# Optimization experiments

Hardware: AMD Instinct MI355X
Metric: run time of the kernel (lower is better)

Reference implementation:

```python
import jax, jax.numpy as jnp
import numpy as np

N_NODES = 50000
N_HEDGES = 50000
NNZ = 1_600_000
IN_CH = 256      # hedge feature dim
OUT_CH = 256
NODE_CH = 128    # node feature dim
Q_CH = 64        # query_channels
NEG_SLOPE = 0.2


def _glorot(key, shape):
    fan_in, fan_out = shape
    lim = np.sqrt(6.0 / (fan_in + fan_out)).astype(np.float32)
    return jax.random.uniform(key, shape, jnp.float32, -lim, lim)


def setup_inputs() -> dict:
    key = jax.random.key(0)
    ks = jax.random.split(key, 10)
    p = jax.random.normal(ks[0], (N_NODES, NODE_CH), jnp.float32)
    q = jax.random.normal(ks[1], (N_HEDGES, IN_CH), jnp.float32)
    node_idx = jax.random.randint(ks[2], (NNZ,), 0, N_NODES)
    hedge_idx = jax.random.randint(ks[3], (NNZ,), 0, N_HEDGES)
    hedge_index = jnp.stack([node_idx, hedge_idx]).astype(jnp.int64)
    w1 = _glorot(ks[4], (IN_CH, NODE_CH))
    w2 = _glorot(ks[5], (IN_CH, Q_CH))
    w3 = _glorot(ks[6], (NODE_CH, Q_CH))
    w4 = _glorot(ks[7], (NODE_CH, OUT_CH))
    w5 = _glorot(ks[8], (NODE_CH, Q_CH))
    w6 = _glorot(ks[9], (IN_CH, Q_CH))
    return {"p": p, "q": q, "hedge_index": hedge_index,
            "w1": w1, "w2": w2, "w3": w3, "w4": w4, "w5": w5, "w6": w6}


def _segment_softmax(scores, seg, num_segments):
    # PyG-style: exp(x - segment_max) / (segment_sum + 1e-16)
    m = jax.lax.stop_gradient(jax.ops.segment_max(scores, seg, num_segments=num_segments))
    ex = jnp.exp(scores - m[seg])
    s = jax.ops.segment_sum(ex, seg, num_segments=num_segments)
    return ex / (s[seg] + 1e-16)


def reference(p, q, hedge_index, w1, w2, w3, w4, w5, w6):
    n_nodes, n_hedges = p.shape[0], q.shape[0]
    node_i = hedge_index[0]   # [E] node ids
    hedge_j = hedge_index[1]  # [E] hedge ids
    scale = 1.0 / np.sqrt(Q_CH).astype(np.float32)

    # --- stage 1: hedge -> node attention ---
    q_p = q @ w1              # [H, node_ch]
    q_pp = q @ w2             # [H, Q]
    q_ppp = p @ w3            # [N, Q]
    e = jax.nn.leaky_relu((q_ppp[node_i] * q_pp[hedge_j]).sum(-1), NEG_SLOPE)
    e = _segment_softmax(e, node_i, n_nodes)
    p_out = jax.ops.segment_sum(scale * e[:, None] * q_p[hedge_j], node_i,
                                num_segments=n_nodes)  # [N, node_ch]

    # --- stage 2: node -> hedge attention ---
    p_p = p_out @ w4          # [N, out_ch]
    p_pp = p_out @ w5         # [N, Q]
    p_ppp = q @ w6            # [H, Q]
    v = jax.nn.leaky_relu((p_pp[node_i] * p_ppp[hedge_j]).sum(-1), NEG_SLOPE)
    v = _segment_softmax(v, hedge_j, n_hedges)
    q_out = jax.ops.segment_sum(scale * v[:, None] * p_p[node_i], hedge_j,
                                num_segments=n_hedges)  # [H, out_ch]
    return q_out
```

## Files before the change

kernel.cpp:

```cpp
#include <hip/hip_runtime.h>
#include <hip/hip_bf16.h>

#define NODE_CH 128
#define IN_CH   256
#define OUT_CH  256
#define Q_CH    64
#define MAXD    256

#define W_BITS 7
#define W_SEG  128
#define MAX_NB 400
#define CAP    4608
#define CHUNK  4096

__device__ __forceinline__ int load_idx(const void* base, long long i, int is64) {
  if (is64) return (int)((const long long*)base)[i];
  return ((const int*)base)[i];
}

__global__ void detect_kernel(const unsigned int* __restrict__ idx, int* __restrict__ flag) {
  if (threadIdx.x == 0 && blockIdx.x == 0) {
    int allz = 1;
    for (int i = 1; i < 32; i += 2) allz &= (idx[i] == 0u);
    *flag = allz;
  }
}

__global__ __launch_bounds__(512) void bin_kernel(
    const void* __restrict__ idx, const int* __restrict__ flagp,
    int* __restrict__ stagingN, int* __restrict__ stagingH,
    int* __restrict__ gbcntN, int* __restrict__ gbcntH,
    long long E, int NBN, int NBH) {
  __shared__ int ni[CHUNK], hj[CHUNK];
  __shared__ int histN[MAX_NB], histH[MAX_NB];
  __shared__ int baseN[MAX_NB], baseH[MAX_NB];
  __shared__ int curN[MAX_NB],  curH[MAX_NB];
  int is64 = *flagp;
  long long e0 = (long long)blockIdx.x * CHUNK;
  int n = (int)((E - e0 < CHUNK) ? (E - e0) : CHUNK);
  for (int i = threadIdx.x; i < n; i += 512) {
    ni[i] = load_idx(idx, e0 + i, is64);
    hj[i] = load_idx(idx, E + e0 + i, is64);
  }
  for (int i = threadIdx.x; i < MAX_NB; i += 512) {
    histN[i] = 0; histH[i] = 0; curN[i] = 0; curH[i] = 0;
  }
  __syncthreads();
  for (int i = threadIdx.x; i < n; i += 512) {
    atomicAdd(&histN[ni[i] >> W_BITS], 1);
    atomicAdd(&histH[hj[i] >> W_BITS], 1);
  }
  __syncthreads();
  for (int b = threadIdx.x; b < NBN; b += 512)
    if (histN[b]) baseN[b] = atomicAdd(&gbcntN[b], histN[b]);
  for (int b = threadIdx.x; b < NBH; b += 512)
    if (histH[b]) baseH[b] = atomicAdd(&gbcntH[b], histH[b]);
  __syncthreads();
  for (int i = threadIdx.x; i < n; i += 512) {
    int v = ni[i], h = hj[i];
    int bn = v >> W_BITS, bh = h >> W_BITS;
    int rn = baseN[bn] + atomicAdd(&curN[bn], 1);
    if (rn < CAP) stagingN[bn * CAP + rn] = ((v & (W_SEG - 1)) << 16) | h;
    int rh = baseH[bh] + atomicAdd(&curH[bh], 1);
    if (rh < CAP) stagingH[bh * CAP + rh] = ((h & (W_SEG - 1)) << 16) | v;
  }
}

__global__ __launch_bounds__(512) void bucket_sort_kernel(
    const int* __restrict__ stagingN, const int* __restrict__ gbcntN,
    int* __restrict__ rowN, int* __restrict__ csrN, int SN, int NBN,
    const int* __restrict__ stagingH, const int* __restrict__ gbcntH,
    int* __restrict__ rowH, int* __restrict__ csrH, int SH, int NBH,
    long long E) {
  int side = blockIdx.y;
  const int* staging = side ? stagingH : stagingN;
  const int* gbcnt   = side ? gbcntH   : gbcntN;
  int* row = side ? rowH : rowN;
  int* csr = side ? csrH : csrN;
  int S  = side ? SH  : SN;
  int NB = side ? NBH : NBN;
  int b = blockIdx.x;
  if (b >= NB) return;

  __shared__ int eLDS[CAP];
  __shared__ int outb[CAP];
  __shared__ int hist[W_SEG], lstart[W_SEG + 1], cnt[W_SEG];
  __shared__ int red[8];
  __shared__ int basesh;

  int n_b = gbcnt[b];
  int nc = (n_b < CAP) ? n_b : CAP;

  int partial = 0;
  for (int i = threadIdx.x; i < b; i += 512) partial += gbcnt[i];
  #pragma unroll
  for (int o = 1; o < 64; o <<= 1) partial += __shfl_xor(partial, o);
  if ((threadIdx.x & 63) == 0) red[threadIdx.x >> 6] = partial;
  for (int i = threadIdx.x; i < W_SEG; i += 512) { hist[i] = 0; cnt[i] = 0; }
  __syncthreads();
  if (threadIdx.x == 0) {
    int s = 0;
    #pragma unroll
    for (int w = 0; w < 8; ++w) s += red[w];
    basesh = s;
  }
  __syncthreads();
  int base = basesh;

  for (int i = threadIdx.x; i < nc; i += 512) {
    int e = staging[b * CAP + i];
    eLDS[i] = e;
    atomicAdd(&hist[e >> 16], 1);
  }
  __syncthreads();
  if (threadIdx.x == 0) {
    int acc = 0;
    for (int s = 0; s < W_SEG; ++s) { lstart[s] = acc; acc += hist[s]; }
    lstart[W_SEG] = acc;
  }
  __syncthreads();
  int s0 = b * W_SEG;
  for (int s = threadIdx.x; s < W_SEG; s += 512)
    if (s0 + s < S) row[s0 + s] = base + lstart[s];
  if (b == NB - 1 && threadIdx.x == 0) row[S] = (int)E;
  __syncthreads();
  for (int i = threadIdx.x; i < nc; i += 512) {
    int e = eLDS[i];
    int s = e >> 16;
    int r = atomicAdd(&cnt[s], 1);
    outb[lstart[s] + r] = e & 0xffff;
  }
  __syncthreads();
  for (int i = threadIdx.x; i < nc; i += 512) csr[base + i] = outb[i];
}

#define GBM 128
#define GBN 64
#define GBK 16

__device__ __forceinline__ unsigned short f2bf(float f) {
  __hip_bfloat16 h = __float2bfloat16(f);
  return *reinterpret_cast<unsigned short*>(&h);
}

__global__ __launch_bounds__(256) void gemm_f32(const float* __restrict__ A,
                                                const float* __restrict__ B,
                                                float* __restrict__ C,
                                                unsigned short* __restrict__ Cb,
                                                int M, int N, int K) {
  __shared__ float As[GBK][GBM + 4];
  __shared__ float Bs[GBK][GBN];
  int tid = threadIdx.x;
  int tx = tid & 15;
  int ty = tid >> 4;
  int row0 = blockIdx.y * GBM;
  int col0 = blockIdx.x * GBN;
  float acc[8][4] = {};
  for (int k0 = 0; k0 < K; k0 += GBK) {
    #pragma unroll
    for (int i = 0; i < 2; ++i) {
      int idx = tid + i * 256;
      int r   = idx >> 2;
      int kq  = (idx & 3) << 2;
      float4 v = make_float4(0.f, 0.f, 0.f, 0.f);
      int gr = row0 + r;
      if (gr < M) v = *(const float4*)&A[(long long)gr * K + k0 + kq];
      As[kq + 0][r] = v.x; As[kq + 1][r] = v.y; As[kq + 2][r] = v.z; As[kq + 3][r] = v.w;
    }
    {
      int kr = tid >> 4;
      int cq = (tid & 15) << 2;
      *(float4*)&Bs[kr][cq] = *(const float4*)&B[(long long)(k0 + kr) * N + col0 + cq];
    }
    __syncthreads();
    #pragma unroll
    for (int kk = 0; kk < GBK; ++kk) {
      float a[8], bb[4];
      *(float4*)&a[0] = *(const float4*)&As[kk][ty * 8];
      *(float4*)&a[4] = *(const float4*)&As[kk][ty * 8 + 4];
      *(float4*)&bb[0] = *(const float4*)&Bs[kk][tx * 4];
      #pragma unroll
      for (int i = 0; i < 8; ++i)
        #pragma unroll
        for (int j = 0; j < 4; ++j)
          acc[i][j] = fmaf(a[i], bb[j], acc[i][j]);
    }
    __syncthreads();
  }
  #pragma unroll
  for (int i = 0; i < 8; ++i) {
    int gr = row0 + ty * 8 + i;
    if (gr < M) {
      if (C)  *(float4*)&C[(long long)gr * N + col0 + tx * 4] = *(float4*)&acc[i][0];
      if (Cb) {
        ushort4 h;
        h.x = f2bf(acc[i][0]); h.y = f2bf(acc[i][1]);
        h.z = f2bf(acc[i][2]); h.w = f2bf(acc[i][3]);
        *(ushort4*)&Cb[(long long)gr * N + col0 + tx * 4] = h;
      }
    }
  }
}

__device__ __forceinline__ float bf_lo(unsigned int u) { return __uint_as_float(u << 16); }
__device__ __forceinline__ float bf_hi(unsigned int u) { return __uint_as_float(u & 0xffff0000u); }

template <int ACC_CH>
__global__ __launch_bounds__(256) void stage_kernel(
    const int* __restrict__ row,
    const int* __restrict__ oth_arr,
    const float* __restrict__ attn_seg,
    const float* __restrict__ attn_oth,
    const unsigned short* __restrict__ valb,
    float* __restrict__ out,
    int n_seg) {
  __shared__ float sc_all[4][MAXD];
  __shared__ int   so_all[4][MAXD];
  int wave = threadIdx.x >> 6;
  int lane = threadIdx.x & 63;
  int seg = blockIdx.x * 4 + wave;
  bool active = (seg < n_seg);
  int segc = active ? seg : 0;
  int beg = row[segc];
  int end = row[segc + 1];
  int cnt = active ? min(end - beg, MAXD) : 0;
  float* sc = sc_all[wave];
  int*   so = so_all[wave];

  int sub = lane >> 4;
  int qi  = lane & 15;
  float4 a = *(const float4*)&attn_seg[(long long)segc * Q_CH + qi * 4];

  float m = -3.402823466e38f;
  for (int g = 0; g < cnt; g += 4) {
    int ei = g + sub;
    float s = 0.f;
    int oth = 0;
    if (ei < cnt) {
      oth = oth_arr[beg + ei];
      float4 b = *(const float4*)&attn_oth[(long long)oth * Q_CH + qi * 4];
      s = a.x * b.x + a.y * b.y + a.z * b.z + a.w * b.w;
    }
    s += __shfl_xor(s, 1); s += __shfl_xor(s, 2);
    s += __shfl_xor(s, 4); s += __shfl_xor(s, 8);
    if (ei < cnt) {
      s = (s > 0.f) ? s : 0.2f * s;
      if (qi == 0) { sc[ei] = s; so[ei] = oth; }
      m = fmaxf(m, s);
    }
  }
  #pragma unroll
  for (int o = 1; o < 64; o <<= 1) m = fmaxf(m, __shfl_xor(m, o));
  __syncthreads();

  float sum = 0.f;
  for (int i = lane; i < cnt; i += 64) {
    float ex = expf(sc[i] - m);
    sc[i] = ex;
    sum += ex;
  }
  #pragma unroll
  for (int o = 1; o < 64; o <<= 1) sum += __shfl_xor(sum, o);
  float inv = 0.125f / (sum + 1e-16f);
  __syncthreads();

  constexpr int VPL = ACC_CH / 64;
  float acc[VPL] = {};
  for (int i = 0; i < cnt; ++i) {
    int oth = so[i];
    float c = sc[i] * inv;
    const unsigned short* vp = &valb[(long long)oth * ACC_CH + lane * VPL];
    if constexpr (VPL == 2) {
      unsigned int u = *(const unsigned int*)vp;
      acc[0] = fmaf(c, bf_lo(u), acc[0]);
      acc[1] = fmaf(c, bf_hi(u), acc[1]);
    } else {
      uint2 u = *(const uint2*)vp;
      acc[0] = fmaf(c, bf_lo(u.x), acc[0]);
      acc[1] = fmaf(c, bf_hi(u.x), acc[1]);
      acc[2] = fmaf(c, bf_lo(u.y), acc[2]);
      acc[3] = fmaf(c, bf_hi(u.y), acc[3]);
    }
  }
  if (active) {
    if constexpr (VPL == 2) {
      *(float2*)&out[(long long)seg * ACC_CH + lane * 2] = make_float2(acc[0], acc[1]);
    } else {
      *(float4*)&out[(long long)seg * ACC_CH + lane * 4] = make_float4(acc[0], acc[1], acc[2], acc[3]);
    }
  }
}

extern "C" void kernel_launch(void* const* d_in, const int* in_sizes, int n_in,
                              void* d_out, int out_size, void* d_ws, size_t ws_size,
                              hipStream_t stream) {
  const float* p  = (const float*)d_in[0];
  const float* q  = (const float*)d_in[1];
  const void*  hidx = d_in[2];
  const float* w1 = (const float*)d_in[3];
  const float* w2 = (const float*)d_in[4];
  const float* w3 = (const float*)d_in[5];
  const float* w4 = (const float*)d_in[6];
  const float* w5 = (const float*)d_in[7];
  const float* w6 = (const float*)d_in[8];

  int nn = in_sizes[0] / NODE_CH;
  int nh = in_sizes[1] / IN_CH;
  long long E = (long long)in_sizes[2] / 2;
  int NBN = (nn + W_SEG - 1) / W_SEG;
  int NBH = (nh + W_SEG - 1) / W_SEG;
  if (NBN > MAX_NB || NBH > MAX_NB || nn > 65536 || nh > 65536) return;

  char* ws = (char*)d_ws;
  size_t off = 0;
  auto alloc = [&](size_t b) { size_t r = off; off += (b + 255) & ~(size_t)255; return r; };
  size_t o_flag  = alloc(4);
  size_t o_rowN  = alloc((size_t)(nn + 1) * 4);
  size_t o_rowH  = alloc((size_t)(nh + 1) * 4);
  size_t o_gbcnt = alloc((size_t)(NBN + NBH) * 4);
  size_t o_pn    = alloc((size_t)E * 4);
  size_t o_ph    = alloc((size_t)E * 4);
  size_t o_qpb   = alloc((size_t)nh * NODE_CH * 2);
  size_t o_qpp   = alloc((size_t)nh * Q_CH * 4);
  size_t o_qppp  = alloc((size_t)nn * Q_CH * 4);
  size_t o_pout  = alloc((size_t)nn * NODE_CH * 4);
  size_t o_ppb   = alloc((size_t)nn * OUT_CH * 2);
  size_t o_ppp2  = o_qpp;
  size_t o_pppp  = o_qppp;
  size_t need_stg = (size_t)MAX_NB * CAP * 4;
  size_t o_stgN = o_qpb;
  size_t o_stgH = o_qpp;
  if ((size_t)nh * NODE_CH * 2 < need_stg) return;
  if ((size_t)nh * Q_CH * 4 < need_stg) return;
  if (off > ws_size) return;

  int* flag   = (int*)(ws + o_flag);
  int* rowN   = (int*)(ws + o_rowN);
  int* rowH   = (int*)(ws + o_rowH);
  int* gbcntN = (int*)(ws + o_gbcnt);
  int* gbcntH = gbcntN + NBN;
  int* pn     = (int*)(ws + o_pn);
  int* ph     = (int*)(ws + o_ph);
  int* stgN   = (int*)(ws + o_stgN);
  int* stgH   = (int*)(ws + o_stgH);
  unsigned short* qpb = (unsigned short*)(ws + o_qpb);
  float* qpp  = (float*)(ws + o_qpp);
  float* qppp = (float*)(ws + o_qppp);
  float* pout = (float*)(ws + o_pout);
  unsigned short* ppb = (unsigned short*)(ws + o_ppb);
  float* ppp2 = (float*)(ws + o_ppp2);
  float* pppp = (float*)(ws + o_pppp);

  hipMemsetAsync(gbcntN, 0, (size_t)(NBN + NBH) * 4, stream);
  detect_kernel<<<1, 64, 0, stream>>>((const unsigned int*)hidx, flag);

  int nblk = (int)((E + CHUNK - 1) / CHUNK);
  bin_kernel<<<nblk, 512, 0, stream>>>(hidx, flag, stgN, stgH, gbcntN, gbcntH, E, NBN, NBH);
  int nbmax = NBN > NBH ? NBN : NBH;
  bucket_sort_kernel<<<dim3(nbmax, 2), 512, 0, stream>>>(
      stgN, gbcntN, rowN, pn, nn, NBN,
      stgH, gbcntH, rowH, ph, nh, NBH, E);

  gemm_f32<<<dim3(NODE_CH / GBN, (nh + GBM - 1) / GBM), 256, 0, stream>>>(q, w1, nullptr, qpb, nh, NODE_CH, IN_CH);
  gemm_f32<<<dim3(Q_CH / GBN,    (nh + GBM - 1) / GBM), 256, 0, stream>>>(q, w2, qpp,  nullptr, nh, Q_CH, IN_CH);
  gemm_f32<<<dim3(Q_CH / GBN,    (nn + GBM - 1) / GBM), 256, 0, stream>>>(p, w3, qppp, nullptr, nn, Q_CH, NODE_CH);

  stage_kernel<NODE_CH><<<(nn + 3) / 4, 256, 0, stream>>>(
      rowN, pn, qppp, qpp, qpb, pout, nn);

  gemm_f32<<<dim3(OUT_CH / GBN, (nn + GBM - 1) / GBM), 256, 0, stream>>>(pout, w4, nullptr, ppb, nn, OUT_CH, NODE_CH);
  gemm_f32<<<dim3(Q_CH / GBN,   (nn + GBM - 1) / GBM), 256, 0, stream>>>(pout, w5, ppp2, nullptr, nn, Q_CH, NODE_CH);
  gemm_f32<<<dim3(Q_CH / GBN,   (nh + GBM - 1) / GBM), 256, 0, stream>>>(q,    w6, pppp, nullptr, nh, Q_CH, IN_CH);

  stage_kernel<OUT_CH><<<(nh + 3) / 4, 256, 0, stream>>>(
      rowH, ph, pppp, ppp2, ppb, (float*)d_out, nh);
}
```

Baseline: 552.1 us.

## Reassociate stage-2 projections and fuse online-softmax gather into single pass

Stage 2 no longer projects p_out through w4 and w5 per node. Each hedge's score vector is instead precomputed as (q@w6)@w5^T, scores are taken directly against the fp16 p_out rows, and w4 is applied after aggregation on the hedge side. Both stage kernels now use a single-pass online softmax with two half-waves and a merge, which removes the LDS score buffers and the MAXD degree cap. Stage 1 reads one packed row per hedge holding the fp32 score part and the fp16 value part. Intermediates move from bf16 to fp16, which changes rounding and overflow range, and one small transpose kernel plus one extra GEMM are added.

```diff
diff --git a/kernel.cpp b/kernel.cpp
--- a/kernel.cpp
+++ b/kernel.cpp
@@ -1,17 +1,30 @@
 #include <hip/hip_runtime.h>
 #include <hip/hip_bf16.h>
+#include <hip/hip_fp16.h>
 
 #define NODE_CH 128
 #define IN_CH   256
 #define OUT_CH  256
 #define Q_CH    64
-#define MAXD    256
 
 #define W_BITS 7
 #define W_SEG  128
 #define MAX_NB 400
 #define CAP    4608
 #define CHUNK  4096
+
+__device__ __forceinline__ float2 h2_to_f2(unsigned int u) {
+  __half2 h; *reinterpret_cast<unsigned int*>(&h) = u;
+  return __half22float2(h);
+}
+__device__ __forceinline__ unsigned int f2_to_h2(float x, float y) {
+  __half2 h = __floats2half2_rn(x, y);
+  return *reinterpret_cast<unsigned int*>(&h);
+}
+__device__ __forceinline__ unsigned short f2h(float f) {
+  __half h = __float2half_rn(f);
+  return *reinterpret_cast<unsigned short*>(&h);
+}
 
 __device__ __forceinline__ int load_idx(const void* base, long long i, int is64) {
   if (is64) return (int)((const long long*)base)[i];
@@ -138,15 +151,11 @@
 #define GBN 64
 #define GBK 16
 
-__device__ __forceinline__ unsigned short f2bf(float f) {
-  __hip_bfloat16 h = __float2bfloat16(f);
-  return *reinterpret_cast<unsigned short*>(&h);
-}
-
 __global__ __launch_bounds__(256) void gemm_f32(const float* __restrict__ A,
                                                 const float* __restrict__ B,
-                                                float* __restrict__ C,
-                                                unsigned short* __restrict__ Cb,
+                                                float* __restrict__ C, int ldc,
+                                                unsigned short* __restrict__ C16,
+                                                int ldc16, int coloff16,
                                                 int M, int N, int K) {
   __shared__ float As[GBK][GBM + 4];
   __shared__ float Bs[GBK][GBN];
@@ -191,103 +200,121 @@
   for (int i = 0; i < 8; ++i) {
     int gr = row0 + ty * 8 + i;
     if (gr < M) {
-      if (C)  *(float4*)&C[(long long)gr * N + col0 + tx * 4] = *(float4*)&acc[i][0];
-      if (Cb) {
+      if (C) *(float4*)&C[(long long)gr * ldc + col0 + tx * 4] = *(float4*)&acc[i][0];
+      if (C16) {
         ushort4 h;
-        h.x = f2bf(acc[i][0]); h.y = f2bf(acc[i][1]);
-        h.z = f2bf(acc[i][2]); h.w = f2bf(acc[i][3]);
-        *(ushort4*)&Cb[(long long)gr * N + col0 + tx * 4] = h;
+        h.x = f2h(acc[i][0]); h.y = f2h(acc[i][1]);
+        h.z = f2h(acc[i][2]); h.w = f2h(acc[i][3]);
+        *(ushort4*)&C16[(long long)gr * ldc16 + coloff16 + col0 + tx * 4] = h;
       }
     }
   }
 }
 
-__device__ __forceinline__ float bf_lo(unsigned int u) { return __uint_as_float(u << 16); }
-__device__ __forceinline__ float bf_hi(unsigned int u) { return __uint_as_float(u & 0xffff0000u); }
-
-template <int ACC_CH>
-__global__ __launch_bounds__(256) void stage_kernel(
-    const int* __restrict__ row,
-    const int* __restrict__ oth_arr,
-    const float* __restrict__ attn_seg,
-    const float* __restrict__ attn_oth,
-    const unsigned short* __restrict__ valb,
+__global__ void transpose_w5(const float* __restrict__ w5, float* __restrict__ w5t) {
+  int t = blockIdx.x * 256 + threadIdx.x;
+  if (t < 128 * 64) { int r = t >> 6, c = t & 63; w5t[c * 128 + r] = w5[r * 64 + c]; }
+}
+
+__global__ __launch_bounds__(256) void stage1_fused(
+    const int* __restrict__ row, const int* __restrict__ oth_arr,
+    const float* __restrict__ segv,
+    const unsigned int* __restrict__ rows,
+    unsigned short* __restrict__ out16,
+    int n_seg) {
+  int wave = threadIdx.x >> 6, lane = threadIdx.x & 63;
+  int seg = blockIdx.x * 4 + wave;
+  if (seg >= n_seg) return;
+  int li = lane & 31;
+  int grp = lane >> 5;
+  int beg = row[seg];
+  int cnt = row[seg + 1] - beg;
+  float2 a = *(const float2*)&segv[(long long)seg * 64 + li * 2];
+  float m = -1e30f, ssum = 0.f;
+  float ax = 0.f, ay = 0.f, az = 0.f, aw = 0.f;
+  for (int ei = grp; ei < cnt; ei += 2) {
+    int o = oth_arr[beg + ei];
+    const unsigned int* rp = rows + (long long)o * 128;
+    float2 sv = *(const float2*)(rp + li * 2);
+    uint2  uv = *(const uint2*)(rp + 64 + li * 2);
+    float part = a.x * sv.x + a.y * sv.y;
+    #pragma unroll
+    for (int d = 1; d < 32; d <<= 1) part += __shfl_xor(part, d);
+    float s = part > 0.f ? part : 0.2f * part;
+    float mn = fmaxf(m, s);
+    float corr = __expf(m - mn);
+    float w = __expf(s - mn);
+    m = mn;
+    ssum = ssum * corr + w;
+    float2 v0 = h2_to_f2(uv.x), v1 = h2_to_f2(uv.y);
+    ax = ax * corr + w * v0.x;  ay = ay * corr + w * v0.y;
+    az = az * corr + w * v1.x;  aw = aw * corr + w * v1.y;
+  }
+  float m2 = __shfl_xor(m, 32);
+  float mm = fmaxf(m, m2);
+  float c1 = __expf(m - mm);
+  float c2 = __expf(m2 - mm);
+  float ssum2 = __shfl_xor(ssum, 32);
+  float tot = ssum * c1 + ssum2 * c2;
+  float bx = __shfl_xor(ax, 32), by = __shfl_xor(ay, 32);
+  float bz = __shfl_xor(az, 32), bw = __shfl_xor(aw, 32);
+  ax = ax * c1 + bx * c2;  ay = ay * c1 + by * c2;
+  az = az * c1 + bz * c2;  aw = aw * c1 + bw * c2;
+  float inv = 0.125f / (tot + 1e-16f);
+  if (lane < 32) {
+    uint2 o2;
+    o2.x = f2_to_h2(ax * inv, ay * inv);
+    o2.y = f2_to_h2(az * inv, aw * inv);
+    *(uint2*)(out16 + (long long)seg * 128 + li * 4) = o2;
+  }
+}
+
+__global__ __launch_bounds__(256) void stage2_fused(
+    const int* __restrict__ row, const int* __restrict__ oth_arr,
+    const float* __restrict__ segv,
+    const unsigned int* __restrict__ rows16,
     float* __restrict__ out,
     int n_seg) {
-  __shared__ float sc_all[4][MAXD];
-  __shared__ int   so_all[4][MAXD];
-  int wave = threadIdx.x >> 6;
-  int lane = threadIdx.x & 63;
+  int wave = threadIdx.x >> 6, lane = threadIdx.x & 63;
   int seg = blockIdx.x * 4 + wave;
-  bool active = (seg < n_seg);
-  int segc = active ? seg : 0;
-  int beg = row[segc];
-  int end = row[segc + 1];
-  int cnt = active ? min(end - beg, MAXD) : 0;
-  float* sc = sc_all[wave];
-  int*   so = so_all[wave];
-
-  int sub = lane >> 4;
-  int qi  = lane & 15;
-  float4 a = *(const float4*)&attn_seg[(long long)segc * Q_CH + qi * 4];
-
-  float m = -3.402823466e38f;
-  for (int g = 0; g < cnt; g += 4) {
-    int ei = g + sub;
-    float s = 0.f;
-    int oth = 0;
-    if (ei < cnt) {
-      oth = oth_arr[beg + ei];
-      float4 b = *(const float4*)&attn_oth[(long long)oth * Q_CH + qi * 4];
-      s = a.x * b.x + a.y * b.y + a.z * b.z + a.w * b.w;
-    }
-    s += __shfl_xor(s, 1); s += __shfl_xor(s, 2);
-    s += __shfl_xor(s, 4); s += __shfl_xor(s, 8);
-    if (ei < cnt) {
-      s = (s > 0.f) ? s : 0.2f * s;
-      if (qi == 0) { sc[ei] = s; so[ei] = oth; }
-      m = fmaxf(m, s);
-    }
-  }
-  #pragma unroll
-  for (int o = 1; o < 64; o <<= 1) m = fmaxf(m, __shfl_xor(m, o));
-  __syncthreads();
-
-  float sum = 0.f;
-  for (int i = lane; i < cnt; i += 64) {
-    float ex = expf(sc[i] - m);
-    sc[i] = ex;
-    sum += ex;
-  }
-  #pragma unroll
-  for (int o = 1; o < 64; o <<= 1) sum += __shfl_xor(sum, o);
-  float inv = 0.125f / (sum + 1e-16f);
-  __syncthreads();
-
-  constexpr int VPL = ACC_CH / 64;
-  float acc[VPL] = {};
-  for (int i = 0; i < cnt; ++i) {
-    int oth = so[i];
-    float c = sc[i] * inv;
-    const unsigned short* vp = &valb[(long long)oth * ACC_CH + lane * VPL];
-    if constexpr (VPL == 2) {
-      unsigned int u = *(const unsigned int*)vp;
-      acc[0] = fmaf(c, bf_lo(u), acc[0]);
-      acc[1] = fmaf(c, bf_hi(u), acc[1]);
-    } else {
-      uint2 u = *(const uint2*)vp;
-      acc[0] = fmaf(c, bf_lo(u.x), acc[0]);
-      acc[1] = fmaf(c, bf_hi(u.x), acc[1]);
-      acc[2] = fmaf(c, bf_lo(u.y), acc[2]);
-      acc[3] = fmaf(c, bf_hi(u.y), acc[3]);
-    }
-  }
-  if (active) {
-    if constexpr (VPL == 2) {
-      *(float2*)&out[(long long)seg * ACC_CH + lane * 2] = make_float2(acc[0], acc[1]);
-    } else {
-      *(float4*)&out[(long long)seg * ACC_CH + lane * 4] = make_float4(acc[0], acc[1], acc[2], acc[3]);
-    }
+  if (seg >= n_seg) return;
+  int li = lane & 31;
+  int grp = lane >> 5;
+  int beg = row[seg];
+  int cnt = row[seg + 1] - beg;
+  float4 a = *(const float4*)&segv[(long long)seg * 128 + li * 4];
+  float m = -1e30f, ssum = 0.f;
+  float ax = 0.f, ay = 0.f, az = 0.f, aw = 0.f;
+  for (int ei = grp; ei < cnt; ei += 2) {
+    int o = oth_arr[beg + ei];
+    uint2 uv = ((const uint2*)(rows16 + (long long)o * 64))[li];
+    float2 v0 = h2_to_f2(uv.x), v1 = h2_to_f2(uv.y);
+    float part = a.x * v0.x + a.y * v0.y + a.z * v1.x + a.w * v1.y;
+    #pragma unroll
+    for (int d = 1; d < 32; d <<= 1) part += __shfl_xor(part, d);
+    float s = part > 0.f ? part : 0.2f * part;
+    float mn = fmaxf(m, s);
+    float corr = __expf(m - mn);
+    float w = __expf(s - mn);
+    m = mn;
+    ssum = ssum * corr + w;
+    ax = ax * corr + w * v0.x;  ay = ay * corr + w * v0.y;
+    az = az * corr + w * v1.x;  aw = aw * corr + w * v1.y;
+  }
+  float m2 = __shfl_xor(m, 32);
+  float mm = fmaxf(m, m2);
+  float c1 = __expf(m - mm);
+  float c2 = __expf(m2 - mm);
+  float ssum2 = __shfl_xor(ssum, 32);
+  float tot = ssum * c1 + ssum2 * c2;
+  float bx = __shfl_xor(ax, 32), by = __shfl_xor(ay, 32);
+  float bz = __shfl_xor(az, 32), bw = __shfl_xor(aw, 32);
+  ax = ax * c1 + bx * c2;  ay = ay * c1 + by * c2;
+  az = az * c1 + bz * c2;  aw = aw * c1 + bw * c2;
+  float inv = 0.125f / (tot + 1e-16f);
+  if (lane < 32) {
+    float4 o4 = make_float4(ax * inv, ay * inv, az * inv, aw * inv);
+    *(float4*)(out + (long long)seg * 128 + li * 4) = o4;
   }
 }
 
@@ -310,6 +337,7 @@
   int NBN = (nn + W_SEG - 1) / W_SEG;
   int NBH = (nh + W_SEG - 1) / W_SEG;
   if (NBN > MAX_NB || NBH > MAX_NB || nn > 65536 || nh > 65536) return;
+  int mx = nn > nh ? nn : nh;
 
   char* ws = (char*)d_ws;
   size_t off = 0;
@@ -318,20 +346,19 @@
   size_t o_rowN  = alloc((size_t)(nn + 1) * 4);
   size_t o_rowH  = alloc((size_t)(nh + 1) * 4);
   size_t o_gbcnt = alloc((size_t)(NBN + NBH) * 4);
+  size_t o_w5t   = alloc((size_t)64 * 128 * 4);
   size_t o_pn    = alloc((size_t)E * 4);
   size_t o_ph    = alloc((size_t)E * 4);
-  size_t o_qpb   = alloc((size_t)nh * NODE_CH * 2);
-  size_t o_qpp   = alloc((size_t)nh * Q_CH * 4);
-  size_t o_qppp  = alloc((size_t)nn * Q_CH * 4);
-  size_t o_pout  = alloc((size_t)nn * NODE_CH * 4);
-  size_t o_ppb   = alloc((size_t)nn * OUT_CH * 2);
-  size_t o_ppp2  = o_qpp;
-  size_t o_pppp  = o_qppp;
+  size_t o_po16  = alloc((size_t)nn * NODE_CH * 2);
+  size_t o_qppp  = alloc((size_t)mx * Q_CH * 4);
+  size_t o_G2    = alloc((size_t)nh * NODE_CH * 4);
+  size_t o_pk1   = alloc((size_t)nh * 128 * 4);
+  size_t o_t2    = o_pk1;
   size_t need_stg = (size_t)MAX_NB * CAP * 4;
-  size_t o_stgN = o_qpb;
-  size_t o_stgH = o_qpp;
-  if ((size_t)nh * NODE_CH * 2 < need_stg) return;
-  if ((size_t)nh * Q_CH * 4 < need_stg) return;
+  size_t o_stgN  = o_pk1;
+  size_t o_stgH  = o_G2;
+  if ((size_t)nh * 128 * 4 < need_stg) return;
+  if ((size_t)nh * NODE_CH * 4 < need_stg) return;
   if (off > ws_size) return;
 
   int* flag   = (int*)(ws + o_flag);
@@ -339,20 +366,21 @@
   int* rowH   = (int*)(ws + o_rowH);
   int* gbcntN = (int*)(ws + o_gbcnt);
   int* gbcntH = gbcntN + NBN;
+  float* w5t  = (float*)(ws + o_w5t);
   int* pn     = (int*)(ws + o_pn);
   int* ph     = (int*)(ws + o_ph);
   int* stgN   = (int*)(ws + o_stgN);
   int* stgH   = (int*)(ws + o_stgH);
-  unsigned short* qpb = (unsigned short*)(ws + o_qpb);
-  float* qpp  = (float*)(ws + o_qpp);
+  unsigned short* po16 = (unsigned short*)(ws + o_po16);
   float* qppp = (float*)(ws + o_qppp);
-  float* pout = (float*)(ws + o_pout);
-  unsigned short* ppb = (unsigned short*)(ws + o_ppb);
-  float* ppp2 = (float*)(ws + o_ppp2);
-  float* pppp = (float*)(ws + o_pppp);
+  float* pppp = qppp;
+  float* G2   = (float*)(ws + o_G2);
+  unsigned int* pk1 = (unsigned int*)(ws + o_pk1);
+  float* t2   = (float*)(ws + o_t2);
 
   hipMemsetAsync(gbcntN, 0, (size_t)(NBN + NBH) * 4, stream);
   detect_kernel<<<1, 64, 0, stream>>>((const unsigned int*)hidx, flag);
+  transpose_w5<<<32, 256, 0, stream>>>(w5, w5t);
 
   int nblk = (int)((E + CHUNK - 1) / CHUNK);
   bin_kernel<<<nblk, 512, 0, stream>>>(hidx, flag, stgN, stgH, gbcntN, gbcntH, E, NBN, NBH);
@@ -361,17 +389,22 @@
       stgN, gbcntN, rowN, pn, nn, NBN,
       stgH, gbcntH, rowH, ph, nh, NBH, E);
 
-  gemm_f32<<<dim3(NODE_CH / GBN, (nh + GBM - 1) / GBM), 256, 0, stream>>>(q, w1, nullptr, qpb, nh, NODE_CH, IN_CH);
-  gemm_f32<<<dim3(Q_CH / GBN,    (nh + GBM - 1) / GBM), 256, 0, stream>>>(q, w2, qpp,  nullptr, nh, Q_CH, IN_CH);
-  gemm_f32<<<dim3(Q_CH / GBN,    (nn + GBM - 1) / GBM), 256, 0, stream>>>(p, w3, qppp, nullptr, nn, Q_CH, NODE_CH);
-
-  stage_kernel<NODE_CH><<<(nn + 3) / 4, 256, 0, stream>>>(
-      rowN, pn, qppp, qpp, qpb, pout, nn);
-
-  gemm_f32<<<dim3(OUT_CH / GBN, (nn + GBM - 1) / GBM), 256, 0, stream>>>(pout, w4, nullptr, ppb, nn, OUT_CH, NODE_CH);
-  gemm_f32<<<dim3(Q_CH / GBN,   (nn + GBM - 1) / GBM), 256, 0, stream>>>(pout, w5, ppp2, nullptr, nn, Q_CH, NODE_CH);
-  gemm_f32<<<dim3(Q_CH / GBN,   (nh + GBM - 1) / GBM), 256, 0, stream>>>(q,    w6, pppp, nullptr, nh, Q_CH, IN_CH);
-
-  stage_kernel<OUT_CH><<<(nh + 3) / 4, 256, 0, stream>>>(
-      rowH, ph, pppp, ppp2, ppb, (float*)d_out, nh);
-}
+  gemm_f32<<<dim3(Q_CH / GBN,    (nh + GBM - 1) / GBM), 256, 0, stream>>>(
+      q, w2, (float*)pk1, 128, nullptr, 0, 0, nh, Q_CH, IN_CH);
+  gemm_f32<<<dim3(NODE_CH / GBN, (nh + GBM - 1) / GBM), 256, 0, stream>>>(
+      q, w1, nullptr, 0, (unsigned short*)pk1, 256, 128, nh, NODE_CH, IN_CH);
+  gemm_f32<<<dim3(Q_CH / GBN,    (nn + GBM - 1) / GBM), 256, 0, stream>>>(
+      p, w3, qppp, Q_CH, nullptr, 0, 0, nn, Q_CH, NODE_CH);
+
+  stage1_fused<<<(nn + 3) / 4, 256, 0, stream>>>(rowN, pn, qppp, pk1, po16, nn);
+
+  gemm_f32<<<dim3(Q_CH / GBN,    (nh + GBM - 1) / GBM), 256, 0, stream>>>(
+      q, w6, pppp, Q_CH, nullptr, 0, 0, nh, Q_CH, IN_CH);
+  gemm_f32<<<dim3(NODE_CH / GBN, (nh + GBM - 1) / GBM), 256, 0, stream>>>(
+      pppp, w5t, G2, NODE_CH, nullptr, 0, 0, nh, NODE_CH, Q_CH);
+
+  stage2_fused<<<(nh + 3) / 4, 256, 0, stream>>>(rowH, ph, G2, (const unsigned int*)po16, t2, nh);
+
+  gemm_f32<<<dim3(OUT_CH / GBN, (nh + GBM - 1) / GBM), 256, 0, stream>>>(
+      t2, w4, (float*)d_out, OUT_CH, nullptr, 0, 0, nh, OUT_CH, NODE_CH);
+}
```

Measured after the change: 511.6 us. -7.3%, faster.
